# Optimization experiments

Hardware: AMD Instinct MI355X
Metric: run time of the kernel (lower is better)

Reference implementation:

```python
import jax, jax.numpy as jnp
import numpy as np

D_MODEL = 768
NUM_HEADS = 12
DEPTH = D_MODEL // NUM_HEADS
HIDDEN = int(D_MODEL * 4.0)
LN_EPS = 1e-5


def layer_norm(x, g, b):
    mu = jnp.mean(x, axis=-1, keepdims=True)
    var = jnp.mean(jnp.square(x - mu), axis=-1, keepdims=True)
    return (x - mu) * jax.lax.rsqrt(var + LN_EPS) * g + b


def setup_inputs() -> dict:
    key = jax.random.key(0)
    ks = jax.random.split(key, 8)
    s = 0.02
    return {
        "x": jax.random.normal(ks[0], (2, 2048, D_MODEL), dtype=jnp.float32),
        "ln1_g": jnp.ones((D_MODEL,), jnp.float32),
        "ln1_b": jnp.zeros((D_MODEL,), jnp.float32),
        "w_qkv": jax.random.normal(ks[1], (D_MODEL, 3 * D_MODEL), jnp.float32) * s,
        "b_qkv": jnp.zeros((3 * D_MODEL,), jnp.float32),
        "w_proj": jax.random.normal(ks[2], (D_MODEL, D_MODEL), jnp.float32) * s,
        "b_proj": jnp.zeros((D_MODEL,), jnp.float32),
        "ln2_g": jnp.ones((D_MODEL,), jnp.float32),
        "ln2_b": jnp.zeros((D_MODEL,), jnp.float32),
        "w1": jax.random.normal(ks[3], (D_MODEL, HIDDEN), jnp.float32) * s,
        "b1": jnp.zeros((HIDDEN,), jnp.float32),
        "w2": jax.random.normal(ks[4], (HIDDEN, D_MODEL), jnp.float32) * s,
        "b2": jnp.zeros((D_MODEL,), jnp.float32),
    }


def reference(x, ln1_g, ln1_b, w_qkv, b_qkv, w_proj, b_proj, ln2_g, ln2_b, w1, b1, w2, b2):
    B, N, C = x.shape
    # --- MHA branch (pre-norm) ---
    h = layer_norm(x, ln1_g, ln1_b)
    qkv = h @ w_qkv + b_qkv                             # [B,N,3C]
    qkv = qkv.reshape(B, N, NUM_HEADS, DEPTH, 3)
    qkv = jnp.transpose(qkv, (4, 0, 2, 1, 3))           # [3,B,H,N,D]
    q, k, v = qkv[0], qkv[1], qkv[2]
    scale = 1.0 / jnp.sqrt(jnp.asarray(DEPTH, x.dtype))
    attn = jnp.einsum('bhnd,bhmd->bhnm', q, k) * scale  # [B,H,N,N]
    attn = jax.nn.softmax(attn, axis=-1)
    o = jnp.einsum('bhnm,bhmd->bhnd', attn, v)          # [B,H,N,D]
    o = jnp.transpose(o, (0, 2, 1, 3)).reshape(B, N, C)
    o = o @ w_proj + b_proj
    x = x + o
    # --- MLP branch (pre-norm) ---
    h = layer_norm(x, ln2_g, ln2_b)
    h = jax.nn.gelu(h @ w1 + b1, approximate=False)
    h = h @ w2 + b2
    return x + h
```

## Files before the change

kernel.cpp:

```cpp
#include <hip/hip_runtime.h>

typedef unsigned short u16;
typedef __attribute__((ext_vector_type(8))) short short8;
typedef __attribute__((ext_vector_type(4))) float float4v;

#define TOK 4096
#define CDIM 768
#define NHEAD 12
#define DHEAD 64
#define HID 3072
#define SEQ 2048
#define BHTOT 24

#define QSCALE 0.18033688011112042f

__device__ __forceinline__ u16 f2bf(float f) {
  unsigned int u = __builtin_bit_cast(unsigned int, f);
  u = (u + 0x7fffu + ((u >> 16) & 1u)) >> 16;
  return (u16)u;
}
__device__ __forceinline__ float bf2f(u16 v) {
  unsigned int u = ((unsigned int)v) << 16;
  return __builtin_bit_cast(float, u);
}

#define GLD16(gaddr, laddr)                                                    \
  __builtin_amdgcn_global_load_lds(                                            \
      (const __attribute__((address_space(1))) unsigned int*)(gaddr),          \
      (__attribute__((address_space(3))) unsigned int*)(laddr), 16, 0, 0)

template <int NCHUNK>
__device__ __forceinline__ void stage_swz(const u16* __restrict__ gbase,
                                          int grs, u16* lds, int tid) {
#pragma unroll
  for (int c = 0; c < NCHUNK; ++c) {
    int off = c * 4096 + tid * 16;
    int row = off >> 7;
    int colb = (off & 127) ^ ((row & 7) << 4);
    GLD16(gbase + (size_t)row * grs + (colb >> 1), (char*)lds + off);
  }
}

__device__ __forceinline__ short8 lds_frag(const u16* lds, int row, int cb) {
  return *(const short8*)((const char*)lds +
                          ((row << 7) | (cb ^ ((row & 7) << 4))));
}

__global__ __launch_bounds__(256) void transpose_cast_all(
    const float* __restrict__ w0, const float* __restrict__ wp,
    const float* __restrict__ wm1, const float* __restrict__ wm2,
    u16* __restrict__ o0, u16* __restrict__ op, u16* __restrict__ om1,
    u16* __restrict__ om2) {
  __shared__ float tile[32][33];
  int t = blockIdx.x;
  const float* in;
  u16* out;
  int K, Nw, ti;
  if (t < 1728) {
    in = w0; out = o0; K = 768; Nw = 2304; ti = t;
  } else if (t < 2304) {
    in = wp; out = op; K = 768; Nw = 768; ti = t - 1728;
  } else if (t < 4608) {
    in = wm1; out = om1; K = 768; Nw = 3072; ti = t - 2304;
  } else {
    in = wm2; out = om2; K = 3072; Nw = 768; ti = t - 4608;
  }
  int ntx = Nw >> 5;
  int n0 = (ti % ntx) * 32, k0 = (ti / ntx) * 32;
  int tx = threadIdx.x, ty = threadIdx.y;
#pragma unroll
  for (int i = 0; i < 4; ++i)
    tile[ty + i * 8][tx] = in[(size_t)(k0 + ty + i * 8) * Nw + n0 + tx];
  __syncthreads();
#pragma unroll
  for (int i = 0; i < 4; ++i)
    out[(size_t)(n0 + ty + i * 8) * K + k0 + tx] = f2bf(tile[tx][ty + i * 8]);
}

template <int IN_BF16>
__global__ __launch_bounds__(256) void ln_kernel(
    const void* __restrict__ xv, const float* __restrict__ gam,
    const float* __restrict__ bet, u16* __restrict__ out) {
  int row = blockIdx.x;
  int t = threadIdx.x;
  float v0, v1, v2;
  if (IN_BF16) {
    const u16* xr = (const u16*)xv + (size_t)row * CDIM;
    v0 = bf2f(xr[t]);
    v1 = bf2f(xr[t + 256]);
    v2 = bf2f(xr[t + 512]);
  } else {
    const float* xr = (const float*)xv + (size_t)row * CDIM;
    v0 = xr[t];
    v1 = xr[t + 256];
    v2 = xr[t + 512];
  }
  float s = v0 + v1 + v2;
  __shared__ float red[16];
  int lane = t & 63, wid = t >> 6;
#pragma unroll
  for (int off = 32; off; off >>= 1) s += __shfl_down(s, off);
  if (lane == 0) red[wid] = s;
  __syncthreads();
  if (t == 0) red[8] = (red[0] + red[1] + red[2] + red[3]) * (1.f / CDIM);
  __syncthreads();
  float mu = red[8];
  float d0 = v0 - mu, d1 = v1 - mu, d2 = v2 - mu;
  float q = d0 * d0 + d1 * d1 + d2 * d2;
#pragma unroll
  for (int off = 32; off; off >>= 1) q += __shfl_down(q, off);
  if (lane == 0) red[4 + wid] = q;
  __syncthreads();
  if (t == 0) {
    float var = (red[4] + red[5] + red[6] + red[7]) * (1.f / CDIM);
    red[9] = rsqrtf(var + 1e-5f);
  }
  __syncthreads();
  float rstd = red[9];
  u16* orow = out + (size_t)row * CDIM;
  orow[t] = f2bf(d0 * rstd * gam[t] + bet[t]);
  orow[t + 256] = f2bf(d1 * rstd * gam[t + 256] + bet[t + 256]);
  orow[t + 512] = f2bf(d2 * rstd * gam[t + 512] + bet[t + 512]);
}

template <int EPI, int BM, int BN, int DB>
__global__ __launch_bounds__(256) void gemm_bt(
    const u16* __restrict__ A, const u16* __restrict__ BT,
    const float* __restrict__ bias, const float* __restrict__ resf,
    const u16* __restrict__ resb, float* __restrict__ outf,
    u16* __restrict__ ob0, u16* __restrict__ ob1, u16* __restrict__ ob2,
    int K) {
  constexpr int MR = BM / 32, NR = BN / 32;
  constexpr int NBUF = DB ? 2 : 1;
  constexpr int NL = BM / 32 + BN / 32;
  __shared__ u16 As[NBUF][BM * 64];
  __shared__ u16 Bs[NBUF][BN * 64];
  int tid = threadIdx.x;
  int gx = gridDim.x;
  int nwg = gx * (int)gridDim.y;
  int flat = blockIdx.y * gx + blockIdx.x;
  int qq = nwg >> 3, rr = nwg & 7;
  int xcd = flat & 7, rest = flat >> 3;
  int swz = (xcd < rr ? xcd * (qq + 1) : rr * (qq + 1) + (xcd - rr) * qq) + rest;
  int row0 = (swz / gx) * BM, col0 = (swz % gx) * BN;
  int wid = tid >> 6, lane = tid & 63;
  int wm = wid >> 1, wn = wid & 1;
  int rbase = wm * (BM / 2), cbase = wn * (BN / 2);
  int r = lane & 15, g = lane >> 4;
  float4v zero = {0.f, 0.f, 0.f, 0.f};
  float4v acc[MR][NR];
#pragma unroll
  for (int m = 0; m < MR; ++m)
#pragma unroll
    for (int n = 0; n < NR; ++n) acc[m][n] = zero;
  const int nk = K >> 6;
  if (DB) {
    stage_swz<BM / 32>(A + (size_t)row0 * K, K, As[0], tid);
    stage_swz<BN / 32>(BT + (size_t)col0 * K, K, Bs[0], tid);
  }
  for (int k = 0; k < nk; ++k) {
    const u16* Ac;
    const u16* Bc;
    if (DB) {
      Ac = As[k & 1];
      Bc = Bs[k & 1];
      if (k + 1 < nk) {
        stage_swz<BM / 32>(A + (size_t)row0 * K + (k + 1) * 64, K,
                           As[(k + 1) & 1], tid);
        stage_swz<BN / 32>(BT + (size_t)col0 * K + (k + 1) * 64, K,
                           Bs[(k + 1) & 1], tid);
        if constexpr (NL == 4)
          asm volatile("s_waitcnt vmcnt(4)" ::: "memory");
        else if constexpr (NL == 6)
          asm volatile("s_waitcnt vmcnt(6)" ::: "memory");
        else
          asm volatile("s_waitcnt vmcnt(0)" ::: "memory");
      } else {
        asm volatile("s_waitcnt vmcnt(0)" ::: "memory");
      }
      __builtin_amdgcn_s_barrier();
    } else {
      Ac = As[0];
      Bc = Bs[0];
      stage_swz<BM / 32>(A + (size_t)row0 * K + k * 64, K, As[0], tid);
      stage_swz<BN / 32>(BT + (size_t)col0 * K + k * 64, K, Bs[0], tid);
      __syncthreads();
    }
#pragma unroll
    for (int kk = 0; kk < 2; ++kk) {
      short8 av[MR], bv[NR];
#pragma unroll
      for (int m = 0; m < MR; ++m)
        av[m] = lds_frag(Ac, rbase + m * 16 + r, kk * 64 + g * 16);
#pragma unroll
      for (int n = 0; n < NR; ++n)
        bv[n] = lds_frag(Bc, cbase + n * 16 + r, kk * 64 + g * 16);
#pragma unroll
      for (int m = 0; m < MR; ++m)
#pragma unroll
        for (int n = 0; n < NR; ++n)
          acc[m][n] = __builtin_amdgcn_mfma_f32_16x16x32_bf16(av[m], bv[n],
                                                              acc[m][n], 0, 0, 0);
    }
    if (DB)
      __builtin_amdgcn_s_barrier();
    else
      __syncthreads();
  }
#pragma unroll
  for (int m = 0; m < MR; ++m) {
#pragma unroll
    for (int n = 0; n < NR; ++n) {
#pragma unroll
      for (int j = 0; j < 4; ++j) {
        int row = row0 + rbase + m * 16 + g * 4 + j;
        int col = col0 + cbase + n * 16 + r;
        float v = acc[m][n][j] + bias[col];
        if (EPI == 0) {
          int sdx = col % 3;
          int hd = col / 3;
          int h = hd >> 6, d = hd & 63;
          int b = row >> 11, nn = row & 2047;
          if (sdx == 0)
            ob0[(((size_t)(b * NHEAD + h) * SEQ + nn) << 6) + d] =
                f2bf(v * QSCALE);
          else if (sdx == 1)
            ob1[(((size_t)(b * NHEAD + h) * SEQ + nn) << 6) + d] = f2bf(v);
          else
            ob2[(((size_t)(b * NHEAD + h) * DHEAD + d) << 11) + nn] = f2bf(v);
        } else if (EPI == 1) {
          ob0[(size_t)row * CDIM + col] =
              f2bf(resf[(size_t)row * CDIM + col] + v);
        } else if (EPI == 3) {
          outf[(size_t)row * CDIM + col] =
              bf2f(resb[(size_t)row * CDIM + col]) + v;
        } else if (EPI == 2) {
          float ge = 0.5f * v * (1.f + erff(v * 0.70710678118f));
          ob0[(size_t)row * HID + col] = f2bf(ge);
        }
      }
    }
  }
}

__global__ __launch_bounds__(256) void attn_kernel(
    const u16* __restrict__ Qb, const u16* __restrict__ Kb,
    const u16* __restrict__ Vt, u16* __restrict__ Op,
    float* __restrict__ ml) {
  __shared__ u16 Ks[2][64 * 64];
  __shared__ u16 Vs[2][64 * 64];
  __shared__ u16 Ps[4][32 * 64];
  int tid = threadIdx.x, wid = tid >> 6, lane = tid & 63;
  int r = lane & 15, g = lane >> 4;
  int bh = blockIdx.y;
  int half = blockIdx.x >> 4, qblk = blockIdx.x & 15;
  const u16* Qh = Qb + (size_t)bh * SEQ * DHEAD;
  const u16* Kh = Kb + (size_t)bh * SEQ * DHEAD + (size_t)half * 1024 * DHEAD;
  const u16* Vh = Vt + (size_t)bh * DHEAD * SEQ + half * 1024;
  int qr0 = qblk * 128 + wid * 32;
  short8 qa[2][2];
#pragma unroll
  for (int qg = 0; qg < 2; ++qg) {
    qa[qg][0] =
        *(const short8*)(&Qh[(size_t)(qr0 + qg * 16 + r) * DHEAD + g * 8]);
    qa[qg][1] =
        *(const short8*)(&Qh[(size_t)(qr0 + qg * 16 + r) * DHEAD + 32 + g * 8]);
  }
  short8 vones;
#pragma unroll
  for (int i = 0; i < 8; ++i) vones[i] = (short)0x3F80;
  float4v zero = {0.f, 0.f, 0.f, 0.f};
  float4v oacc[2][4];
  float4v accsum[2];
#pragma unroll
  for (int qg = 0; qg < 2; ++qg) {
    accsum[qg] = zero;
#pragma unroll
    for (int nd = 0; nd < 4; ++nd) oacc[qg][nd] = zero;
  }
  u16* Pw = &Ps[wid][0];
  stage_swz<2>(Kh, DHEAD, Ks[0], tid);
  stage_swz<2>(Vh, SEQ, Vs[0], tid);
  __syncthreads();
  for (int t0 = 0; t0 < 1024; t0 += 64) {
    int cur = (t0 >> 6) & 1;
    const u16* Kc = Ks[cur];
    const u16* Vc = Vs[cur];
    if (t0 + 64 < 1024) {
      stage_swz<2>(Kh + (size_t)(t0 + 64) * DHEAD, DHEAD, Ks[cur ^ 1], tid);
      stage_swz<2>(Vh + (t0 + 64), SEQ, Vs[cur ^ 1], tid);
    }
    float4v s[2][4];
#pragma unroll
    for (int qg = 0; qg < 2; ++qg)
#pragma unroll
      for (int n = 0; n < 4; ++n) s[qg][n] = zero;
#pragma unroll
    for (int kk = 0; kk < 2; ++kk) {
      short8 av[4];
#pragma unroll
      for (int n = 0; n < 4; ++n)
        av[n] = lds_frag(Kc, n * 16 + r, kk * 64 + g * 16);
      __builtin_amdgcn_s_setprio(1);
#pragma unroll
      for (int qg = 0; qg < 2; ++qg)
#pragma unroll
        for (int n = 0; n < 4; ++n)
          s[qg][n] = __builtin_amdgcn_mfma_f32_16x16x32_bf16(
              av[n], qa[qg][kk], s[qg][n], 0, 0, 0);
      __builtin_amdgcn_s_setprio(0);
    }
#pragma unroll
    for (int qg = 0; qg < 2; ++qg) {
#pragma unroll
      for (int n = 0; n < 4; ++n) {
        float p[4];
#pragma unroll
        for (int j = 0; j < 4; ++j) {
          float e = s[qg][n][j];
          asm("v_exp_f32 %0, %1" : "=v"(p[j]) : "v"(e));
        }
        unsigned int wlo, whi;
        asm("v_cvt_pk_bf16_f32 %0, %1, %2" : "=v"(wlo) : "v"(p[0]), "v"(p[1]));
        asm("v_cvt_pk_bf16_f32 %0, %1, %2" : "=v"(whi) : "v"(p[2]), "v"(p[3]));
        uint2 w2;
        w2.x = wlo;
        w2.y = whi;
        *(uint2*)((char*)Pw + qg * 2048 +
                  ((r << 7) | ((n * 32 + g * 8) ^ ((r & 7) << 4)))) = w2;
      }
    }
#pragma unroll
    for (int kk = 0; kk < 2; ++kk) {
      short8 bv[4];
#pragma unroll
      for (int nd = 0; nd < 4; ++nd)
        bv[nd] = lds_frag(Vc, nd * 16 + r, kk * 64 + g * 16);
      short8 pa[2];
#pragma unroll
      for (int qg = 0; qg < 2; ++qg)
        pa[qg] = lds_frag(Pw + qg * 1024, r, kk * 64 + g * 16);
      __builtin_amdgcn_s_setprio(1);
#pragma unroll
      for (int qg = 0; qg < 2; ++qg) {
#pragma unroll
        for (int nd = 0; nd < 4; ++nd)
          oacc[qg][nd] = __builtin_amdgcn_mfma_f32_16x16x32_bf16(
              pa[qg], bv[nd], oacc[qg][nd], 0, 0, 0);
        accsum[qg] = __builtin_amdgcn_mfma_f32_16x16x32_bf16(
            pa[qg], vones, accsum[qg], 0, 0, 0);
      }
      __builtin_amdgcn_s_setprio(0);
    }
    __syncthreads();
  }
  size_t obase = ((size_t)(half * BHTOT + bh) * SEQ);
#pragma unroll
  for (int qg = 0; qg < 2; ++qg) {
#pragma unroll
    for (int nd = 0; nd < 4; ++nd)
#pragma unroll
      for (int j = 0; j < 4; ++j) {
        int rowq = qr0 + qg * 16 + g * 4 + j;
        Op[(obase + rowq) * DHEAD + nd * 16 + r] = f2bf(oacc[qg][nd][j]);
      }
    if (r == 0) {
#pragma unroll
      for (int j = 0; j < 4; ++j) {
        int rowq = qr0 + qg * 16 + g * 4 + j;
        ml[obase + rowq] = accsum[qg][j];
      }
    }
  }
}

__global__ __launch_bounds__(256) void attn_combine(
    const u16* __restrict__ Op, const float* __restrict__ ml,
    u16* __restrict__ aO) {
  int t = threadIdx.x;
  int idx = blockIdx.x * 4 + (t >> 6);
  int d = t & 63;
  int bh = idx >> 11, row = idx & 2047;
  int b = bh / NHEAD, h = bh - b * NHEAD;
  float l0 = ml[idx];
  float l1 = ml[(size_t)BHTOT * SEQ + idx];
  float o0 = bf2f(Op[(size_t)idx * DHEAD + d]);
  float o1 = bf2f(Op[((size_t)BHTOT * SEQ + idx) * DHEAD + d]);
  float val = (o0 + o1) / (l0 + l1);
  aO[(size_t)(b * SEQ + row) * CDIM + h * DHEAD + d] = f2bf(val);
}

extern "C" void kernel_launch(void* const* d_in, const int* in_sizes, int n_in,
                              void* d_out, int out_size, void* d_ws,
                              size_t ws_size, hipStream_t stream) {
  const float* x = (const float*)d_in[0];
  const float* ln1g = (const float*)d_in[1];
  const float* ln1b = (const float*)d_in[2];
  const float* wqkv = (const float*)d_in[3];
  const float* bqkv = (const float*)d_in[4];
  const float* wproj = (const float*)d_in[5];
  const float* bproj = (const float*)d_in[6];
  const float* ln2g = (const float*)d_in[7];
  const float* ln2b = (const float*)d_in[8];
  const float* w1 = (const float*)d_in[9];
  const float* b1 = (const float*)d_in[10];
  const float* w2 = (const float*)d_in[11];
  const float* b2 = (const float*)d_in[12];
  float* out = (float*)d_out;

  char* ws = (char*)d_ws;
  size_t o = 0;
  auto nxt = [&](size_t bytes) -> void* {
    void* p = ws + o;
    o += (bytes + 255) & ~(size_t)255;
    return p;
  };
  u16* wqkvT = (u16*)nxt((size_t)2304 * 768 * 2);
  u16* wprojT = (u16*)nxt((size_t)768 * 768 * 2);
  u16* w1T = (u16*)nxt((size_t)3072 * 768 * 2);
  u16* w2T = (u16*)nxt((size_t)768 * 3072 * 2);
  u16* h1 = (u16*)nxt((size_t)TOK * CDIM * 2);
  u16* Qb = (u16*)nxt((size_t)TOK * CDIM * 2);
  u16* Kb = (u16*)nxt((size_t)TOK * CDIM * 2);
  u16* Vt = (u16*)nxt((size_t)TOK * CDIM * 2);
  u16* aO = (u16*)nxt((size_t)TOK * CDIM * 2);
  u16* y1b = (u16*)nxt((size_t)TOK * CDIM * 2);
  u16* h2 = (u16*)nxt((size_t)TOK * CDIM * 2);
  u16* mh = (u16*)nxt((size_t)TOK * HID * 2);
  float* ml = (float*)nxt((size_t)2 * BHTOT * SEQ * 4);
  u16* Op = (u16*)mh;

  transpose_cast_all<<<6912, dim3(32, 8), 0, stream>>>(
      wqkv, wproj, w1, w2, wqkvT, wprojT, w1T, w2T);

  ln_kernel<0><<<TOK, 256, 0, stream>>>(x, ln1g, ln1b, h1);

  gemm_bt<0, 128, 96, 0><<<dim3(2304 / 96, TOK / 128), 256, 0, stream>>>(
      h1, wqkvT, bqkv, nullptr, nullptr, nullptr, Qb, Kb, Vt, 768);

  attn_kernel<<<dim3(32, BHTOT), 256, 0, stream>>>(Qb, Kb, Vt, Op, ml);
  attn_combine<<<BHTOT * SEQ / 4, 256, 0, stream>>>(Op, ml, aO);

  gemm_bt<1, 64, 64, 1><<<dim3(768 / 64, TOK / 64), 256, 0, stream>>>(
      aO, wprojT, bproj, x, nullptr, nullptr, y1b, nullptr, nullptr, 768);

  ln_kernel<1><<<TOK, 256, 0, stream>>>(y1b, ln2g, ln2b, h2);

  gemm_bt<2, 128, 64, 1><<<dim3(3072 / 64, TOK / 128), 256, 0, stream>>>(
      h2, w1T, b1, nullptr, nullptr, nullptr, mh, nullptr, nullptr, 768);

  gemm_bt<3, 64, 64, 1><<<dim3(768 / 64, TOK / 64), 256, 0, stream>>>(
      mh, w2T, b2, nullptr, y1b, out, nullptr, nullptr, nullptr, 3072);
}
```

Before: 172.9 us.

## Merge weight cast with first layernorm; add triple-buffered prefetch for 64x64 GEMMs

The weight transpose-cast and the first layernorm now run as one launch, each block picking its role from its block index, which saves one kernel launch and the gap between them. The GEMM template gains a DB=2 mode with three LDS buffers that prefetch two K-tiles ahead. Waitcnt values are adjusted so more loads stay in flight. The output-projection and MLP-down GEMMs switch to this mode, which hides more global-memory latency at the cost of extra LDS and possibly lower occupancy.

```diff
diff --git a/kernel.cpp b/kernel.cpp
--- a/kernel.cpp
+++ b/kernel.cpp
@@ -46,55 +46,79 @@
                           ((row << 7) | (cb ^ ((row & 7) << 4))));
 }
 
-__global__ __launch_bounds__(256) void transpose_cast_all(
+__global__ __launch_bounds__(256) void prologue_kernel(
     const float* __restrict__ w0, const float* __restrict__ wp,
     const float* __restrict__ wm1, const float* __restrict__ wm2,
     u16* __restrict__ o0, u16* __restrict__ op, u16* __restrict__ om1,
-    u16* __restrict__ om2) {
+    u16* __restrict__ om2, const float* __restrict__ x,
+    const float* __restrict__ gam, const float* __restrict__ bet,
+    u16* __restrict__ h1) {
   __shared__ float tile[32][33];
-  int t = blockIdx.x;
-  const float* in;
-  u16* out;
-  int K, Nw, ti;
-  if (t < 1728) {
-    in = w0; out = o0; K = 768; Nw = 2304; ti = t;
-  } else if (t < 2304) {
-    in = wp; out = op; K = 768; Nw = 768; ti = t - 1728;
-  } else if (t < 4608) {
-    in = wm1; out = om1; K = 768; Nw = 3072; ti = t - 2304;
-  } else {
-    in = wm2; out = om2; K = 3072; Nw = 768; ti = t - 4608;
-  }
-  int ntx = Nw >> 5;
-  int n0 = (ti % ntx) * 32, k0 = (ti / ntx) * 32;
-  int tx = threadIdx.x, ty = threadIdx.y;
-#pragma unroll
-  for (int i = 0; i < 4; ++i)
-    tile[ty + i * 8][tx] = in[(size_t)(k0 + ty + i * 8) * Nw + n0 + tx];
-  __syncthreads();
-#pragma unroll
-  for (int i = 0; i < 4; ++i)
-    out[(size_t)(n0 + ty + i * 8) * K + k0 + tx] = f2bf(tile[tx][ty + i * 8]);
-}
-
-template <int IN_BF16>
-__global__ __launch_bounds__(256) void ln_kernel(
-    const void* __restrict__ xv, const float* __restrict__ gam,
+  __shared__ float red[16];
+  int t = threadIdx.x;
+  int blk = blockIdx.x;
+  if (blk < 6912) {
+    const float* in;
+    u16* out;
+    int K, Nw, ti;
+    if (blk < 1728) {
+      in = w0; out = o0; K = 768; Nw = 2304; ti = blk;
+    } else if (blk < 2304) {
+      in = wp; out = op; K = 768; Nw = 768; ti = blk - 1728;
+    } else if (blk < 4608) {
+      in = wm1; out = om1; K = 768; Nw = 3072; ti = blk - 2304;
+    } else {
+      in = wm2; out = om2; K = 3072; Nw = 768; ti = blk - 4608;
+    }
+    int ntx = Nw >> 5;
+    int n0 = (ti % ntx) * 32, k0 = (ti / ntx) * 32;
+    int tx = t & 31, ty = t >> 5;
+#pragma unroll
+    for (int i = 0; i < 4; ++i)
+      tile[ty + i * 8][tx] = in[(size_t)(k0 + ty + i * 8) * Nw + n0 + tx];
+    __syncthreads();
+#pragma unroll
+    for (int i = 0; i < 4; ++i)
+      out[(size_t)(n0 + ty + i * 8) * K + k0 + tx] = f2bf(tile[tx][ty + i * 8]);
+    return;
+  }
+  int row = blk - 6912;
+  const float* xr = x + (size_t)row * CDIM;
+  float v0 = xr[t], v1 = xr[t + 256], v2 = xr[t + 512];
+  float s = v0 + v1 + v2;
+  int lane = t & 63, wid = t >> 6;
+#pragma unroll
+  for (int off = 32; off; off >>= 1) s += __shfl_down(s, off);
+  if (lane == 0) red[wid] = s;
+  __syncthreads();
+  if (t == 0) red[8] = (red[0] + red[1] + red[2] + red[3]) * (1.f / CDIM);
+  __syncthreads();
+  float mu = red[8];
+  float d0 = v0 - mu, d1 = v1 - mu, d2 = v2 - mu;
+  float q = d0 * d0 + d1 * d1 + d2 * d2;
+#pragma unroll
+  for (int off = 32; off; off >>= 1) q += __shfl_down(q, off);
+  if (lane == 0) red[4 + wid] = q;
+  __syncthreads();
+  if (t == 0) {
+    float var = (red[4] + red[5] + red[6] + red[7]) * (1.f / CDIM);
+    red[9] = rsqrtf(var + 1e-5f);
+  }
+  __syncthreads();
+  float rstd = red[9];
+  u16* orow = h1 + (size_t)row * CDIM;
+  orow[t] = f2bf(d0 * rstd * gam[t] + bet[t]);
+  orow[t + 256] = f2bf(d1 * rstd * gam[t + 256] + bet[t + 256]);
+  orow[t + 512] = f2bf(d2 * rstd * gam[t + 512] + bet[t + 512]);
+}
+
+__global__ __launch_bounds__(256) void ln_kernel_b(
+    const u16* __restrict__ xv, const float* __restrict__ gam,
     const float* __restrict__ bet, u16* __restrict__ out) {
   int row = blockIdx.x;
   int t = threadIdx.x;
-  float v0, v1, v2;
-  if (IN_BF16) {
-    const u16* xr = (const u16*)xv + (size_t)row * CDIM;
-    v0 = bf2f(xr[t]);
-    v1 = bf2f(xr[t + 256]);
-    v2 = bf2f(xr[t + 512]);
-  } else {
-    const float* xr = (const float*)xv + (size_t)row * CDIM;
-    v0 = xr[t];
-    v1 = xr[t + 256];
-    v2 = xr[t + 512];
-  }
+  const u16* xr = xv + (size_t)row * CDIM;
+  float v0 = bf2f(xr[t]), v1 = bf2f(xr[t + 256]), v2 = bf2f(xr[t + 512]);
   float s = v0 + v1 + v2;
   __shared__ float red[16];
   int lane = t & 63, wid = t >> 6;
@@ -131,7 +155,7 @@
     u16* __restrict__ ob0, u16* __restrict__ ob1, u16* __restrict__ ob2,
     int K) {
   constexpr int MR = BM / 32, NR = BN / 32;
-  constexpr int NBUF = DB ? 2 : 1;
+  constexpr int NBUF = (DB == 0) ? 1 : (DB == 1 ? 2 : 3);
   constexpr int NL = BM / 32 + BN / 32;
   __shared__ u16 As[NBUF][BM * 64];
   __shared__ u16 Bs[NBUF][BN * 64];
@@ -154,25 +178,37 @@
 #pragma unroll
     for (int n = 0; n < NR; ++n) acc[m][n] = zero;
   const int nk = K >> 6;
-  if (DB) {
+  if (DB >= 1) {
     stage_swz<BM / 32>(A + (size_t)row0 * K, K, As[0], tid);
     stage_swz<BN / 32>(BT + (size_t)col0 * K, K, Bs[0], tid);
+    if (DB == 2 && nk > 1) {
+      stage_swz<BM / 32>(A + (size_t)row0 * K + 64, K, As[1], tid);
+      stage_swz<BN / 32>(BT + (size_t)col0 * K + 64, K, Bs[1], tid);
+    }
   }
   for (int k = 0; k < nk; ++k) {
     const u16* Ac;
     const u16* Bc;
-    if (DB) {
-      Ac = As[k & 1];
-      Bc = Bs[k & 1];
-      if (k + 1 < nk) {
-        stage_swz<BM / 32>(A + (size_t)row0 * K + (k + 1) * 64, K,
-                           As[(k + 1) & 1], tid);
-        stage_swz<BN / 32>(BT + (size_t)col0 * K + (k + 1) * 64, K,
-                           Bs[(k + 1) & 1], tid);
+    if (DB >= 1) {
+      Ac = As[k % NBUF];
+      Bc = Bs[k % NBUF];
+      int nx = (DB == 1) ? k + 1 : k + 2;
+      if (nx < nk) {
+        stage_swz<BM / 32>(A + (size_t)row0 * K + nx * 64, K, As[nx % NBUF],
+                           tid);
+        stage_swz<BN / 32>(BT + (size_t)col0 * K + nx * 64, K, Bs[nx % NBUF],
+                           tid);
+        if constexpr (DB * NL == 4)
+          asm volatile("s_waitcnt vmcnt(4)" ::: "memory");
+        else if constexpr (DB * NL == 6)
+          asm volatile("s_waitcnt vmcnt(6)" ::: "memory");
+        else if constexpr (DB * NL == 8)
+          asm volatile("s_waitcnt vmcnt(8)" ::: "memory");
+        else
+          asm volatile("s_waitcnt vmcnt(0)" ::: "memory");
+      } else if (DB == 2 && k + 1 < nk) {
         if constexpr (NL == 4)
           asm volatile("s_waitcnt vmcnt(4)" ::: "memory");
-        else if constexpr (NL == 6)
-          asm volatile("s_waitcnt vmcnt(6)" ::: "memory");
         else
           asm volatile("s_waitcnt vmcnt(0)" ::: "memory");
       } else {
@@ -202,7 +238,7 @@
           acc[m][n] = __builtin_amdgcn_mfma_f32_16x16x32_bf16(av[m], bv[n],
                                                               acc[m][n], 0, 0, 0);
     }
-    if (DB)
+    if (DB >= 1)
       __builtin_amdgcn_s_barrier();
     else
       __syncthreads();
@@ -430,10 +466,9 @@
   float* ml = (float*)nxt((size_t)2 * BHTOT * SEQ * 4);
   u16* Op = (u16*)mh;
 
-  transpose_cast_all<<<6912, dim3(32, 8), 0, stream>>>(
-      wqkv, wproj, w1, w2, wqkvT, wprojT, w1T, w2T);
-
-  ln_kernel<0><<<TOK, 256, 0, stream>>>(x, ln1g, ln1b, h1);
+  prologue_kernel<<<11008, 256, 0, stream>>>(wqkv, wproj, w1, w2, wqkvT,
+                                             wprojT, w1T, w2T, x, ln1g, ln1b,
+                                             h1);
 
   gemm_bt<0, 128, 96, 0><<<dim3(2304 / 96, TOK / 128), 256, 0, stream>>>(
       h1, wqkvT, bqkv, nullptr, nullptr, nullptr, Qb, Kb, Vt, 768);
@@ -441,14 +476,14 @@
   attn_kernel<<<dim3(32, BHTOT), 256, 0, stream>>>(Qb, Kb, Vt, Op, ml);
   attn_combine<<<BHTOT * SEQ / 4, 256, 0, stream>>>(Op, ml, aO);
 
-  gemm_bt<1, 64, 64, 1><<<dim3(768 / 64, TOK / 64), 256, 0, stream>>>(
+  gemm_bt<1, 64, 64, 2><<<dim3(768 / 64, TOK / 64), 256, 0, stream>>>(
       aO, wprojT, bproj, x, nullptr, nullptr, y1b, nullptr, nullptr, 768);
 
-  ln_kernel<1><<<TOK, 256, 0, stream>>>(y1b, ln2g, ln2b, h2);
+  ln_kernel_b<<<TOK, 256, 0, stream>>>(y1b, ln2g, ln2b, h2);
 
   gemm_bt<2, 128, 64, 1><<<dim3(3072 / 64, TOK / 128), 256, 0, stream>>>(
       h2, w1T, b1, nullptr, nullptr, nullptr, mh, nullptr, nullptr, 768);
 
-  gemm_bt<3, 64, 64, 1><<<dim3(768 / 64, TOK / 64), 256, 0, stream>>>(
+  gemm_bt<3, 64, 64, 2><<<dim3(768 / 64, TOK / 64), 256, 0, stream>>>(
       mh, w2T, b2, nullptr, y1b, out, nullptr, nullptr, nullptr, 3072);
 }
```

Measured after the change: 170.1 us. About the same (-1.6%).
